# Kernel optimization log

Hardware: AMD Instinct MI355X
Metric: run time of the kernel (lower is better)

The kernel has to match this reference:

```python
import jax, jax.numpy as jnp
import numpy as np

T, B, IN, H, OUT, L = 2048, 16, 72, 256, 90, 2


def setup_inputs() -> dict:
    key = jax.random.key(0)
    ks = jax.random.split(key, 12)
    s = 0.05
    x = jax.random.normal(ks[0], (T, B, IN), jnp.float32)
    lengths = jnp.clip(jax.random.randint(ks[1], (B,), 1, T + 1), 1, T)
    W1 = jax.random.normal(ks[2], (H, IN), jnp.float32) * s
    b1 = jax.random.normal(ks[3], (H,), jnp.float32) * s
    Wih = jax.random.normal(ks[4], (L, 4 * H, H), jnp.float32) * s
    Whh = jax.random.normal(ks[5], (L, 4 * H, H), jnp.float32) * s
    bih = jax.random.normal(ks[6], (L, 4 * H), jnp.float32) * s
    bhh = jax.random.normal(ks[7], (L, 4 * H), jnp.float32) * s
    W2 = jax.random.normal(ks[8], (OUT, H), jnp.float32) * s
    b2 = jax.random.normal(ks[9], (OUT,), jnp.float32) * s
    return dict(x=x, lengths=lengths, W1=W1, b1=b1, Wih=Wih, Whh=Whh,
                bih=bih, bhh=bhh, W2=W2, b2=b2)


def _lstm_layer(x, mask, Wih, Whh, bih, bhh):
    # x: [T,B,H], mask: [T,B] bool (True = valid frame)
    Hh = Whh.shape[1]
    Bsz = x.shape[1]
    # input projection for all timesteps at once (the only big GEMM)
    gi = jnp.einsum('tbi,gi->tbg', x, Wih) + bih  # [T,B,4H]

    def step(carry, inp):
        h, c = carry
        g_in, m = inp
        g = g_in + h @ Whh.T + bhh
        i, f, gg, o = jnp.split(g, 4, axis=-1)  # PyTorch gate order i,f,g,o
        c_new = jax.nn.sigmoid(f) * c + jax.nn.sigmoid(i) * jnp.tanh(gg)
        h_new = jax.nn.sigmoid(o) * jnp.tanh(c_new)
        m2 = m[:, None]
        # pack semantics: state frozen past each sequence's length, output zero
        h = jnp.where(m2, h_new, h)
        c = jnp.where(m2, c_new, c)
        return (h, c), jnp.where(m2, h_new, jnp.zeros_like(h_new))

    init = (jnp.zeros((Bsz, Hh), x.dtype), jnp.zeros((Bsz, Hh), x.dtype))
    _, ys = jax.lax.scan(step, init, (gi, mask))
    return ys


def reference(x, lengths, W1, b1, Wih, Whh, bih, bhh, W2, b2):
    # linear1 + relu (dropout=0 -> identity)
    h = jax.nn.relu(jnp.einsum('tbi,hi->tbh', x, W1) + b1)
    mask = jnp.arange(T)[:, None] < lengths[None, :]  # [T,B]
    for l in range(L):
        h = _lstm_layer(h, mask, Wih[l], Whh[l], bih[l], bhh[l])
    y = jnp.einsum('tbh,oh->tbo', h, W2) + b2
    # zero out padded frames (they are discarded by the per-sequence slicing)
    return jnp.where(mask[:, :, None], y, jnp.zeros_like(y))
```

## Files before the change

### kernel.cpp

```cpp
#include <hip/hip_runtime.h>
#include <hip/hip_bf16.h>

#define T_STEPS 2048
#define HID 256
#define INF 72
#define OUTF 90
#define HSTR 528

typedef __attribute__((ext_vector_type(4))) float f32x4;
typedef __attribute__((ext_vector_type(8))) short s16x8;
typedef unsigned long long u64;

__device__ __forceinline__ unsigned short f2bf(float f) {
  union { float f; unsigned u; } v; v.f = f;
  unsigned r = (v.u + 0x7FFFu + ((v.u >> 16) & 1u)) >> 16;
  return (unsigned short)r;
}
__device__ __forceinline__ float bf2f(unsigned short s) {
  union { unsigned u; float f; } v; v.u = ((unsigned)s) << 16;
  return v.f;
}
__device__ __forceinline__ float sigm(float x) {
  return __builtin_amdgcn_rcpf(1.f + __builtin_amdgcn_exp2f(-1.44269504f * x));
}
__device__ __forceinline__ float tanh_f(float x) {
  return 1.f - 2.f * __builtin_amdgcn_rcpf(1.f + __builtin_amdgcn_exp2f(2.88539008f * x));
}

__device__ __forceinline__ u64 ld64(const u64* p) {
  return __hip_atomic_load(p, __ATOMIC_RELAXED, __HIP_MEMORY_SCOPE_AGENT);
}
__device__ __forceinline__ void st64(u64* p, u64 v) {
  __hip_atomic_store(p, v, __ATOMIC_RELAXED, __HIP_MEMORY_SCOPE_AGENT);
}
__device__ __forceinline__ void stflag(unsigned* p, unsigned v) {
  __hip_atomic_store(p, v, __ATOMIC_RELAXED, __HIP_MEMORY_SCOPE_AGENT);
}
__device__ __forceinline__ unsigned ldflag(const unsigned* p) {
  return __hip_atomic_load(p, __ATOMIC_RELAXED, __HIP_MEMORY_SCOPE_AGENT);
}
__device__ __forceinline__ void waitflag(const unsigned* p, unsigned target) {
  while (ldflag(p) < target) __builtin_amdgcn_s_sleep(1);
}
__device__ __forceinline__ unsigned wait2(const unsigned* creds, unsigned target, unsigned cred) {
  const u64* cp = (const u64*)creds;
  while (cred < target) {
    u64 v = ld64(cp);
    unsigned a = (unsigned)v, b = (unsigned)(v >> 32);
    cred = a < b ? a : b;
    if (cred < target) __builtin_amdgcn_s_sleep(2);
  }
  return cred;
}
__device__ __forceinline__ s16x8 ld16B_sc1(const unsigned short* p) {
  union { u64 u[2]; s16x8 v; } x;
  const u64* q = (const u64*)p;
  x.u[0] = ld64(q); x.u[1] = ld64(q + 1);
  return x.v;
}
template <int ROLE> __device__ __forceinline__ void ld_g(const unsigned short* p, s16x8& a, s16x8& b) {
  if constexpr (ROLE == 0) { a = *(const s16x8*)p; b = *(const s16x8*)(p + 8); }
  else {
    union { u64 u[2]; s16x8 v; } x, y;
    const u64* q = (const u64*)p;
    x.u[0] = ld64(q); x.u[1] = ld64(q + 1);
    y.u[0] = ld64(q + 2); y.u[1] = ld64(q + 3);
    a = x.v; b = y.v;
  }
}

__global__ __launch_bounds__(256) void inproj(const float* __restrict__ x,
                                              const float* __restrict__ W1,
                                              const float* __restrict__ b1,
                                              float* __restrict__ h0) {
  __shared__ float w1s[HID][INF + 1];
  __shared__ float xs[16][INF];
  const int tid = threadIdx.x;
  const int r0 = blockIdx.x * 16;
  for (int i = tid; i < HID * INF; i += 256) w1s[i / INF][i % INF] = W1[i];
  for (int i = tid; i < 16 * INF; i += 256)
    xs[i / INF][i % INF] = x[(size_t)(r0 + i / INF) * INF + (i % INF)];
  __syncthreads();
  const float bj = b1[tid];
  for (int r = 0; r < 16; ++r) {
    float acc = bj;
#pragma unroll 8
    for (int k = 0; k < INF; ++k) acc += xs[r][k] * w1s[tid][k];
    h0[(size_t)(r0 + r) * HID + tid] = fmaxf(acc, 0.f);
  }
}

__global__ __launch_bounds__(256) void wpack(const float* __restrict__ w,
                                             unsigned short* __restrict__ o) {
  const size_t i = ((size_t)blockIdx.x * 256 + threadIdx.x) * 8;
  f32x4 a = *(const f32x4*)(w + i);
  f32x4 b = *(const f32x4*)(w + i + 4);
  s16x8 v;
#pragma unroll
  for (int e = 0; e < 4; ++e) { v[e] = (short)f2bf(a[e]); v[4 + e] = (short)f2bf(b[e]); }
  *(s16x8*)(o + i) = v;
}

__global__ __launch_bounds__(256) void gi_mfma(const float* __restrict__ h,
                                               const unsigned short* __restrict__ wb,
                                               const float* __restrict__ bih,
                                               const float* __restrict__ bhh,
                                               unsigned short* __restrict__ gi) {
  __shared__ __align__(16) char hs[16 * HSTR];
  __shared__ float bs[1024];
  const int tid = threadIdx.x;
  const int t = blockIdx.x;
  const int lane = tid & 63;
  const int wg = tid >> 6;
  const int j = lane & 15;
  const int hi = lane >> 4;
  for (int i = tid; i < 1024; i += 256) bs[i] = bih[i] + bhh[i];
  {
    const int row = tid >> 4;
    const int c0 = (tid & 15) * 16;
    const float* src = h + ((size_t)t * 16 + row) * 256 + c0;
    f32x4 v0 = *(const f32x4*)(src);
    f32x4 v1 = *(const f32x4*)(src + 4);
    f32x4 v2 = *(const f32x4*)(src + 8);
    f32x4 v3 = *(const f32x4*)(src + 12);
    s16x8 p0, p1;
#pragma unroll
    for (int e = 0; e < 4; ++e) {
      p0[e] = (short)f2bf(v0[e]); p0[4 + e] = (short)f2bf(v1[e]);
      p1[e] = (short)f2bf(v2[e]); p1[4 + e] = (short)f2bf(v3[e]);
    }
    *(s16x8*)(hs + row * HSTR + c0 * 2) = p0;
    *(s16x8*)(hs + row * HSTR + c0 * 2 + 16) = p1;
  }
  __syncthreads();
  const int hread = j * HSTR + hi * 16;
  f32x4 acc[4][4] = {};
#pragma unroll
  for (int kt = 0; kt < 8; ++kt) {
    const int k = kt * 32 + hi * 8;
    const s16x8 a = *(const s16x8*)(hs + hread + kt * 64);
#pragma unroll
    for (int ug2 = 0; ug2 < 4; ++ug2)
#pragma unroll
      for (int q = 0; q < 4; ++q) {
        const s16x8 bw = *(const s16x8*)(wb + (((size_t)(q << 8) + wg * 64 + ug2 * 16 + j) << 8) + k);
        acc[ug2][q] = __builtin_amdgcn_mfma_f32_16x16x32_bf16(bw, a, acc[ug2][q], 0, 0, 0);
      }
  }
#pragma unroll
  for (int ug2 = 0; ug2 < 4; ++ug2) {
    const int sw = wg * 4 + ug2;
    const int uT = sw * 16 + hi * 4;
    s16x8 o0, o1;
#pragma unroll
    for (int r = 0; r < 4; ++r) {
      o0[r]     = (short)f2bf(acc[ug2][0][r] + bs[uT + r]);
      o0[4 + r] = (short)f2bf(acc[ug2][1][r] + bs[256 + uT + r]);
      o1[r]     = (short)f2bf(acc[ug2][2][r] + bs[512 + uT + r]);
      o1[4 + r] = (short)f2bf(acc[ug2][3][r] + bs[768 + uT + r]);
    }
    unsigned short* dst = gi + ((size_t)(t * 16 + sw) * 64 + lane) * 16;
    *(s16x8*)(dst) = o0;
    *(s16x8*)(dst + 8) = o1;
  }
}


template <int ROLE>
__device__ __forceinline__ void scan_tp(
    const unsigned short* __restrict__ gi,
    const unsigned short* __restrict__ whbL,
    const int* __restrict__ lengths,
    unsigned short* __restrict__ hb1,
    float* __restrict__ hout,
    unsigned short* hx,
    unsigned* myflag, unsigned* peerflag,
    unsigned* mycred,
    unsigned* creds,
    int half)
{
  __shared__ __align__(16) char hl[4 * 8192];
  const int tid  = threadIdx.x;
  const int lane = tid & 63;
  const int w    = tid >> 6;
  const int j    = lane & 15;
  const int hi   = lane >> 4;
  const int uB   = half * 128 + w * 16;
  const int myu  = uB + hi * 4;

  s16x8 wfr[32];
#pragma unroll
  for (int kt = 0; kt < 8; ++kt)
#pragma unroll
    for (int q = 0; q < 4; ++q)
      wfr[kt * 4 + q] =
          *(const s16x8*)(whbL + ((size_t)(q * 256 + uB + j) << 8) + kt * 32 + hi * 8);

  const int len = lengths[j];
  float c[4] = {};
  unsigned short hprev[4] = {};

  const int lws = ((j << 9) + (myu << 1)) ^ ((j & 7) << 4);
  *(u64*)(hl + lws) = 0;
  st64((u64*)hx + ((j * 256 + myu) >> 2), 0);
  asm volatile("s_waitcnt vmcnt(0) lgkmcnt(0)" ::: "memory");
  __builtin_amdgcn_s_barrier();
  if (tid == 0) stflag(myflag, 1u);

  const unsigned short* gp = gi + ((size_t)(half * 8 + w) * 64 + lane) * 16;
  unsigned cred = 0;
  if (ROLE == 1) cred = wait2(creds, 8u, cred);
  s16x8 gE0, gE1, gO0, gO1;
  ld_g<ROLE>(gp, gE0, gE1);
  ld_g<ROLE>(gp + 16384, gO0, gO1);

  const int pbase = (1 - half) * 128;

  for (int tg = 0; tg < T_STEPS; tg += 4) {
    if (ROLE == 1) {
      const unsigned target = (tg + 8 <= T_STEPS) ? (unsigned)(tg + 8) : (unsigned)T_STEPS;
      cred = wait2(creds, target, cred);
    }
#pragma unroll
    for (int ts = 0; ts < 4; ++ts) {
      const int t = tg + ts;
      s16x8& g0 = (ts & 1) ? gO0 : gE0;
      s16x8& g1 = (ts & 1) ? gO1 : gE1;
      const int cur = t & 3, nxt = (t + 1) & 3;

      waitflag(peerflag, (unsigned)(t + 1));

      s16x8 avp[4];
#pragma unroll
      for (int p = 0; p < 4; ++p) {
        const int k = pbase + p * 32 + hi * 8;
        avp[p] = ld16B_sc1(hx + cur * 4096 + j * 256 + k);
      }
      s16x8 avo[4];
#pragma unroll
      for (int p = 0; p < 4; ++p) {
        const int k = half * 128 + p * 32 + hi * 8;
        const int off = cur * 8192 + (((j << 9) + (k << 1)) ^ ((j & 7) << 4));
        avo[p] = *(const s16x8*)(hl + off);
      }

      f32x4 acc[4];
#pragma unroll
      for (int r = 0; r < 4; ++r) {
        acc[0][r] = bf2f((unsigned short)g0[r]);
        acc[1][r] = bf2f((unsigned short)g0[4 + r]);
        acc[2][r] = bf2f((unsigned short)g1[r]);
        acc[3][r] = bf2f((unsigned short)g1[4 + r]);
      }
#pragma unroll
      for (int kt = 0; kt < 8; ++kt) {
        const s16x8 a = ((kt >> 2) == half) ? avo[kt & 3] : avp[kt & 3];
#pragma unroll
        for (int q = 0; q < 4; ++q)
          acc[q] = __builtin_amdgcn_mfma_f32_16x16x32_bf16(wfr[kt * 4 + q], a, acc[q], 0, 0, 0);
      }

      u64 hpk = 0, ypk = 0;
      f32x4 yv;
      const bool m = t < len;
#pragma unroll
      for (int r = 0; r < 4; ++r) {
        const float i_  = sigm(acc[0][r]);
        const float f_  = sigm(acc[1][r]);
        const float tg_ = tanh_f(acc[2][r]);
        const float o_  = sigm(acc[3][r]);
        const float cn = f_ * c[r] + i_ * tg_;
        const float hv = o_ * tanh_f(cn);
        c[r] = m ? cn : c[r];
        const unsigned short hb = m ? f2bf(hv) : hprev[r];
        hprev[r] = hb;
        hpk |= (u64)hb << (16 * r);
        if (ROLE == 0) ypk |= (u64)(m ? hb : (unsigned short)0) << (16 * r);
        else           yv[r] = m ? hv : 0.f;
      }
      *(u64*)(hl + nxt * 8192 + lws) = hpk;
      st64((u64*)hx + ((nxt * 4096 + j * 256 + myu) >> 2), hpk);
      asm volatile("s_waitcnt vmcnt(0) lgkmcnt(0)" ::: "memory");
      __builtin_amdgcn_s_barrier();
      if (tid == 0) stflag(myflag, (unsigned)(t + 2));
      if (ROLE == 0) st64((u64*)hb1 + (((size_t)t * 4096 + j * 256 + myu) >> 2), ypk);
      else           *(f32x4*)(hout + ((size_t)t * 16 + j) * 256 + myu) = yv;
      {
        const int tn = (t + 2 < T_STEPS) ? t + 2 : T_STEPS - 1;
        ld_g<ROLE>(gp + (size_t)tn * 16384, g0, g1);
      }
    }
    if (ROLE == 0) {
      asm volatile("s_waitcnt vmcnt(0)" ::: "memory");
      __builtin_amdgcn_s_barrier();
      if (tid == 0) stflag(mycred, (unsigned)(tg + 4));
    }
  }
}

__device__ __forceinline__ void gi2b(int cu,
    const unsigned short* __restrict__ hb1,
    const unsigned short* __restrict__ wb2,
    const float* __restrict__ bih2, const float* __restrict__ bhh2,
    unsigned short* __restrict__ gf2,
    unsigned* creds_in, unsigned* mycred)
{
  const int tid = threadIdx.x;
  const int lane = tid & 63;
  const int w = tid >> 6;
  const int j = lane & 15;
  const int hi = lane >> 4;
  const int sw = cu * 8 + w;

  s16x8 wfr[32];
  float bsum[4][4];
#pragma unroll
  for (int kt = 0; kt < 8; ++kt)
#pragma unroll
    for (int q = 0; q < 4; ++q)
      wfr[kt * 4 + q] =
          *(const s16x8*)(wb2 + ((size_t)(q * 256 + sw * 16 + j) << 8) + kt * 32 + hi * 8);
#pragma unroll
  for (int q = 0; q < 4; ++q)
#pragma unroll
    for (int r = 0; r < 4; ++r) {
      const int col = q * 256 + sw * 16 + hi * 4 + r;
      bsum[q][r] = bih2[col] + bhh2[col];
    }

  unsigned cred = 0;
  for (int tg = 0; tg < T_STEPS; tg += 4) {
    cred = wait2(creds_in, (unsigned)(tg + 4), cred);
#pragma unroll
    for (int ts = 0; ts < 4; ++ts) {
      const int t = tg + ts;
      const unsigned short* ab = hb1 + (size_t)t * 4096 + j * 256 + hi * 8;
      s16x8 av[8];
#pragma unroll
      for (int kt = 0; kt < 8; ++kt) av[kt] = ld16B_sc1(ab + kt * 32);
      f32x4 acc[4];
#pragma unroll
      for (int q = 0; q < 4; ++q)
#pragma unroll
        for (int r = 0; r < 4; ++r) acc[q][r] = bsum[q][r];
#pragma unroll
      for (int kt = 0; kt < 8; ++kt)
#pragma unroll
        for (int q = 0; q < 4; ++q)
          acc[q] = __builtin_amdgcn_mfma_f32_16x16x32_bf16(wfr[kt * 4 + q], av[kt], acc[q], 0, 0, 0);
      u64 p0 = 0, q0 = 0, p1 = 0, q1 = 0;
#pragma unroll
      for (int r = 0; r < 4; ++r) {
        p0 |= (u64)f2bf(acc[0][r]) << (16 * r);
        q0 |= (u64)f2bf(acc[1][r]) << (16 * r);
        p1 |= (u64)f2bf(acc[2][r]) << (16 * r);
        q1 |= (u64)f2bf(acc[3][r]) << (16 * r);
      }
      u64* dst = (u64*)gf2 + ((size_t)(t * 16 + sw) * 64 + lane) * 4;
      st64(dst, p0); st64(dst + 1, q0); st64(dst + 2, p1); st64(dst + 3, q1);
    }
    asm volatile("s_waitcnt vmcnt(0)" ::: "memory");
    __builtin_amdgcn_s_barrier();
    if (tid == 0) stflag(mycred, (unsigned)(tg + 4));
  }
}

__global__ __launch_bounds__(512, 2) void fused_pipe(
    const unsigned short* __restrict__ gf1,
    const unsigned short* __restrict__ whb,
    const unsigned short* __restrict__ wb,
    const float* __restrict__ bih, const float* __restrict__ bhh,
    const int* __restrict__ lengths,
    unsigned short* hb1, unsigned short* gf2, float* hout2,
    unsigned short* hx1, unsigned short* hx2, unsigned* sync)
{
  const int bid = blockIdx.x;
  if (bid == 0)
    scan_tp<0>(gf1, whb, lengths, hb1, nullptr, hx1, sync + 0, sync + 1, sync + 8, nullptr, 0);
  else if (bid == 1)
    scan_tp<0>(gf1, whb, lengths, hb1, nullptr, hx1, sync + 1, sync + 0, sync + 9, nullptr, 1);
  else if (bid == 2)
    gi2b(0, hb1, wb + 262144, bih + 1024, bhh + 1024, gf2, sync + 8, sync + 12);
  else if (bid == 3)
    gi2b(1, hb1, wb + 262144, bih + 1024, bhh + 1024, gf2, sync + 8, sync + 13);
  else if (bid == 4)
    scan_tp<1>(gf2, whb + 262144, lengths, nullptr, hout2, hx2, sync + 2, sync + 3, nullptr, sync + 12, 0);
  else
    scan_tp<1>(gf2, whb + 262144, lengths, nullptr, hout2, hx2, sync + 3, sync + 2, nullptr, sync + 12, 1);
}

__global__ __launch_bounds__(256) void outproj(const float* __restrict__ h2,
                                               const float* __restrict__ W2,
                                               const float* __restrict__ b2,
                                               const int* __restrict__ lengths,
                                               float* __restrict__ y) {
  __shared__ float w2s[OUTF][HID + 1];
  __shared__ float hs[8][HID + 1];
  const int tid = threadIdx.x;
  const int r0 = blockIdx.x * 8;
  for (int i = tid; i < OUTF * HID; i += 256) w2s[i / HID][i % HID] = W2[i];
  for (int i = tid; i < 8 * HID; i += 256)
    hs[i / HID][i % HID] = h2[(size_t)(r0 + i / HID) * HID + (i % HID)];
  __syncthreads();
  for (int oi = tid; oi < 8 * OUTF; oi += 256) {
    const int r = oi / OUTF, o = oi % OUTF;
    const int row = r0 + r, t = row >> 4, b = row & 15;
    float acc = b2[o];
#pragma unroll 8
    for (int k = 0; k < HID; ++k) acc += hs[r][k] * w2s[o][k];
    y[(size_t)row * OUTF + o] = (t < lengths[b]) ? acc : 0.f;
  }
}

extern "C" void kernel_launch(void* const* d_in, const int* in_sizes, int n_in,
                              void* d_out, int out_size, void* d_ws, size_t ws_size,
                              hipStream_t stream) {
  const float* x      = (const float*)d_in[0];
  const int*   lengths= (const int*)d_in[1];
  const float* W1     = (const float*)d_in[2];
  const float* b1     = (const float*)d_in[3];
  const float* Wih    = (const float*)d_in[4];
  const float* Whh    = (const float*)d_in[5];
  const float* bih    = (const float*)d_in[6];
  const float* bhh    = (const float*)d_in[7];
  const float* W2     = (const float*)d_in[8];
  const float* b2     = (const float*)d_in[9];
  float* out = (float*)d_out;

  char* ws = (char*)d_ws;
  float*          h0   = (float*)(ws);
  unsigned short* gf1  = (unsigned short*)(ws + 33554432);
  unsigned short* hb1  = (unsigned short*)(ws + 100663296);
  unsigned short* gf2  = (unsigned short*)(ws + 117440512);
  float*          h2o  = (float*)(ws + 184549376);
  unsigned short* wb   = (unsigned short*)(ws + 218103808);
  unsigned short* whb  = (unsigned short*)(ws + 219152384);
  unsigned short* hx1  = (unsigned short*)(ws + 220200960);
  unsigned short* hx2  = (unsigned short*)(ws + 220233728);
  unsigned*       sync = (unsigned*)(ws + 220266496);

  wpack<<<256, 256, 0, stream>>>(Wih, wb);
  wpack<<<256, 256, 0, stream>>>(Whh, whb);
  inproj<<<2048, 256, 0, stream>>>(x, W1, b1, h0);
  gi_mfma<<<2048, 256, 0, stream>>>(h0, wb, bih, bhh, gf1);

  hipMemsetAsync((void*)hx1, 0, 2 * 32768 + 1024, stream);
  fused_pipe<<<6, 512, 0, stream>>>(gf1, whb, wb, bih, bhh, lengths,
                                    hb1, gf2, h2o, hx1, hx2, sync);

  outproj<<<4096, 256, 0, stream>>>(h2o, W2, b2, lengths, out);
}
```

Measured before the change: 9.317 ms.

## Replace per-step flag handshake with tagged hidden-state exchange between scan blocks

The two blocks that split each LSTM layer's hidden units no longer signal each step with a flag store and poll. Each 32-bit pair of bf16 h values is now stored alongside a 32-bit timestep tag in one 64-bit atomic word, and the consumer polls the data itself until all tags match. It computes the local half of the recurrent matmul from LDS before spinning on the peer half, and issues the next gate-input prefetch earlier. This removes the per-step global store drain and flag round trip, at the cost of doubling exchange buffer size and traffic and relying on 64-bit store atomicity.

```diff
diff --git a/kernel.cpp b/kernel.cpp
--- a/kernel.cpp
+++ b/kernel.cpp
@@ -35,12 +35,6 @@
 }
 __device__ __forceinline__ void stflag(unsigned* p, unsigned v) {
   __hip_atomic_store(p, v, __ATOMIC_RELAXED, __HIP_MEMORY_SCOPE_AGENT);
-}
-__device__ __forceinline__ unsigned ldflag(const unsigned* p) {
-  return __hip_atomic_load(p, __ATOMIC_RELAXED, __HIP_MEMORY_SCOPE_AGENT);
-}
-__device__ __forceinline__ void waitflag(const unsigned* p, unsigned target) {
-  while (ldflag(p) < target) __builtin_amdgcn_s_sleep(1);
 }
 __device__ __forceinline__ unsigned wait2(const unsigned* creds, unsigned target, unsigned cred) {
   const u64* cp = (const u64*)creds;
@@ -52,21 +46,8 @@
   }
   return cred;
 }
-__device__ __forceinline__ s16x8 ld16B_sc1(const unsigned short* p) {
-  union { u64 u[2]; s16x8 v; } x;
-  const u64* q = (const u64*)p;
-  x.u[0] = ld64(q); x.u[1] = ld64(q + 1);
-  return x.v;
-}
-template <int ROLE> __device__ __forceinline__ void ld_g(const unsigned short* p, s16x8& a, s16x8& b) {
-  if constexpr (ROLE == 0) { a = *(const s16x8*)p; b = *(const s16x8*)(p + 8); }
-  else {
-    union { u64 u[2]; s16x8 v; } x, y;
-    const u64* q = (const u64*)p;
-    x.u[0] = ld64(q); x.u[1] = ld64(q + 1);
-    y.u[0] = ld64(q + 2); y.u[1] = ld64(q + 3);
-    a = x.v; b = y.v;
-  }
+__device__ __forceinline__ void ld_g(const unsigned short* p, s16x8& a, s16x8& b) {
+  a = *(const s16x8*)p; b = *(const s16x8*)(p + 8);
 }
 
 __global__ __launch_bounds__(256) void inproj(const float* __restrict__ x,
@@ -173,8 +154,7 @@
     const int* __restrict__ lengths,
     unsigned short* __restrict__ hb1,
     float* __restrict__ hout,
-    unsigned short* hx,
-    unsigned* myflag, unsigned* peerflag,
+    u64* hx,
     unsigned* mycred,
     unsigned* creds,
     int half)
@@ -202,17 +182,15 @@
 
   const int lws = ((j << 9) + (myu << 1)) ^ ((j & 7) << 4);
   *(u64*)(hl + lws) = 0;
-  st64((u64*)hx + ((j * 256 + myu) >> 2), 0);
-  asm volatile("s_waitcnt vmcnt(0) lgkmcnt(0)" ::: "memory");
+  asm volatile("s_waitcnt lgkmcnt(0)" ::: "memory");
   __builtin_amdgcn_s_barrier();
-  if (tid == 0) stflag(myflag, 1u);
 
   const unsigned short* gp = gi + ((size_t)(half * 8 + w) * 64 + lane) * 16;
   unsigned cred = 0;
   if (ROLE == 1) cred = wait2(creds, 8u, cred);
   s16x8 gE0, gE1, gO0, gO1;
-  ld_g<ROLE>(gp, gE0, gE1);
-  ld_g<ROLE>(gp + 16384, gO0, gO1);
+  ld_g(gp, gE0, gE1);
+  ld_g(gp + 16384, gO0, gO1);
 
   const int pbase = (1 - half) * 128;
 
@@ -228,22 +206,6 @@
       s16x8& g1 = (ts & 1) ? gO1 : gE1;
       const int cur = t & 3, nxt = (t + 1) & 3;
 
-      waitflag(peerflag, (unsigned)(t + 1));
-
-      s16x8 avp[4];
-#pragma unroll
-      for (int p = 0; p < 4; ++p) {
-        const int k = pbase + p * 32 + hi * 8;
-        avp[p] = ld16B_sc1(hx + cur * 4096 + j * 256 + k);
-      }
-      s16x8 avo[4];
-#pragma unroll
-      for (int p = 0; p < 4; ++p) {
-        const int k = half * 128 + p * 32 + hi * 8;
-        const int off = cur * 8192 + (((j << 9) + (k << 1)) ^ ((j & 7) << 4));
-        avo[p] = *(const s16x8*)(hl + off);
-      }
-
       f32x4 acc[4];
 #pragma unroll
       for (int r = 0; r < 4; ++r) {
@@ -252,12 +214,52 @@
         acc[2][r] = bf2f((unsigned short)g1[r]);
         acc[3][r] = bf2f((unsigned short)g1[4 + r]);
       }
-#pragma unroll
-      for (int kt = 0; kt < 8; ++kt) {
-        const s16x8 a = ((kt >> 2) == half) ? avo[kt & 3] : avp[kt & 3];
+      {
+        const int tn = (t + 2 < T_STEPS) ? t + 2 : T_STEPS - 1;
+        ld_g(gp + (size_t)tn * 16384, g0, g1);
+      }
+
+#pragma unroll
+      for (int p = 0; p < 4; ++p) {
+        const int kt = half * 4 + p;
+        const int k = half * 128 + p * 32 + hi * 8;
+        const int off = cur * 8192 + (((j << 9) + (k << 1)) ^ ((j & 7) << 4));
+        const s16x8 a = *(const s16x8*)(hl + off);
 #pragma unroll
         for (int q = 0; q < 4; ++q)
           acc[q] = __builtin_amdgcn_mfma_f32_16x16x32_bf16(wfr[kt * 4 + q], a, acc[q], 0, 0, 0);
+      }
+
+      s16x8 avp[4];
+      {
+        const unsigned tagexp = (unsigned)t;
+        for (;;) {
+          bool ok = true;
+#pragma unroll
+          for (int p = 0; p < 4; ++p) {
+            const int k = pbase + p * 32 + hi * 8;
+            const u64* src = hx + (size_t)cur * 2048 + j * 128 + (k >> 1);
+            const u64 a0 = ld64(src), a1 = ld64(src + 1);
+            const u64 a2 = ld64(src + 2), a3 = ld64(src + 3);
+            ok &= ((unsigned)(a0 >> 32) == tagexp) & ((unsigned)(a1 >> 32) == tagexp) &
+                  ((unsigned)(a2 >> 32) == tagexp) & ((unsigned)(a3 >> 32) == tagexp);
+            s16x8 v;
+            v[0] = (short)a0; v[1] = (short)(a0 >> 16);
+            v[2] = (short)a1; v[3] = (short)(a1 >> 16);
+            v[4] = (short)a2; v[5] = (short)(a2 >> 16);
+            v[6] = (short)a3; v[7] = (short)(a3 >> 16);
+            avp[p] = v;
+          }
+          if (__ballot((int)ok) == ~0ull) break;
+          __builtin_amdgcn_s_sleep(1);
+        }
+      }
+#pragma unroll
+      for (int p = 0; p < 4; ++p) {
+        const int kt = (1 - half) * 4 + p;
+#pragma unroll
+        for (int q = 0; q < 4; ++q)
+          acc[q] = __builtin_amdgcn_mfma_f32_16x16x32_bf16(wfr[kt * 4 + q], avp[p], acc[q], 0, 0, 0);
       }
 
       u64 hpk = 0, ypk = 0;
@@ -279,21 +281,24 @@
         else           yv[r] = m ? hv : 0.f;
       }
       *(u64*)(hl + nxt * 8192 + lws) = hpk;
-      st64((u64*)hx + ((nxt * 4096 + j * 256 + myu) >> 2), hpk);
-      asm volatile("s_waitcnt vmcnt(0) lgkmcnt(0)" ::: "memory");
-      __builtin_amdgcn_s_barrier();
-      if (tid == 0) stflag(myflag, (unsigned)(t + 2));
+      {
+        const u64 tag = (u64)(unsigned)(t + 1) << 32;
+        u64* dst = hx + (size_t)nxt * 2048 + j * 128 + (myu >> 1);
+        st64(dst,     (hpk & 0xFFFFFFFFull) | tag);
+        st64(dst + 1, (hpk >> 32)           | tag);
+      }
       if (ROLE == 0) st64((u64*)hb1 + (((size_t)t * 4096 + j * 256 + myu) >> 2), ypk);
       else           *(f32x4*)(hout + ((size_t)t * 16 + j) * 256 + myu) = yv;
-      {
-        const int tn = (t + 2 < T_STEPS) ? t + 2 : T_STEPS - 1;
-        ld_g<ROLE>(gp + (size_t)tn * 16384, g0, g1);
-      }
-    }
-    if (ROLE == 0) {
-      asm volatile("s_waitcnt vmcnt(0)" ::: "memory");
-      __builtin_amdgcn_s_barrier();
-      if (tid == 0) stflag(mycred, (unsigned)(tg + 4));
+
+      if (ROLE == 0 && ts == 3) {
+        asm volatile("s_waitcnt vmcnt(0) lgkmcnt(0)" ::: "memory");
+        __builtin_amdgcn_s_barrier();
+        if (tid == 0) stflag(mycred, (unsigned)(tg + 4));
+      } else {
+        asm volatile("s_waitcnt lgkmcnt(0)" ::: "memory");
+        __builtin_amdgcn_s_barrier();
+      }
+      asm volatile("" ::: "memory");
     }
   }
 }
@@ -337,7 +342,7 @@
       const unsigned short* ab = hb1 + (size_t)t * 4096 + j * 256 + hi * 8;
       s16x8 av[8];
 #pragma unroll
-      for (int kt = 0; kt < 8; ++kt) av[kt] = ld16B_sc1(ab + kt * 32);
+      for (int kt = 0; kt < 8; ++kt) av[kt] = *(const s16x8*)(ab + kt * 32);
       f32x4 acc[4];
 #pragma unroll
       for (int q = 0; q < 4; ++q)
@@ -372,21 +377,21 @@
     const float* __restrict__ bih, const float* __restrict__ bhh,
     const int* __restrict__ lengths,
     unsigned short* hb1, unsigned short* gf2, float* hout2,
-    unsigned short* hx1, unsigned short* hx2, unsigned* sync)
+    u64* hx1, u64* hx2, unsigned* sync)
 {
   const int bid = blockIdx.x;
   if (bid == 0)
-    scan_tp<0>(gf1, whb, lengths, hb1, nullptr, hx1, sync + 0, sync + 1, sync + 8, nullptr, 0);
+    scan_tp<0>(gf1, whb, lengths, hb1, nullptr, hx1, sync + 8, nullptr, 0);
   else if (bid == 1)
-    scan_tp<0>(gf1, whb, lengths, hb1, nullptr, hx1, sync + 1, sync + 0, sync + 9, nullptr, 1);
+    scan_tp<0>(gf1, whb, lengths, hb1, nullptr, hx1, sync + 9, nullptr, 1);
   else if (bid == 2)
     gi2b(0, hb1, wb + 262144, bih + 1024, bhh + 1024, gf2, sync + 8, sync + 12);
   else if (bid == 3)
     gi2b(1, hb1, wb + 262144, bih + 1024, bhh + 1024, gf2, sync + 8, sync + 13);
   else if (bid == 4)
-    scan_tp<1>(gf2, whb + 262144, lengths, nullptr, hout2, hx2, sync + 2, sync + 3, nullptr, sync + 12, 0);
+    scan_tp<1>(gf2, whb + 262144, lengths, nullptr, hout2, hx2, nullptr, sync + 12, 0);
   else
-    scan_tp<1>(gf2, whb + 262144, lengths, nullptr, hout2, hx2, sync + 3, sync + 2, nullptr, sync + 12, 1);
+    scan_tp<1>(gf2, whb + 262144, lengths, nullptr, hout2, hx2, nullptr, sync + 12, 1);
 }
 
 __global__ __launch_bounds__(256) void outproj(const float* __restrict__ h2,
@@ -435,16 +440,16 @@
   float*          h2o  = (float*)(ws + 184549376);
   unsigned short* wb   = (unsigned short*)(ws + 218103808);
   unsigned short* whb  = (unsigned short*)(ws + 219152384);
-  unsigned short* hx1  = (unsigned short*)(ws + 220200960);
-  unsigned short* hx2  = (unsigned short*)(ws + 220233728);
-  unsigned*       sync = (unsigned*)(ws + 220266496);
+  u64*            hx1  = (u64*)(ws + 220200960);
+  u64*            hx2  = (u64*)(ws + 220266496);
+  unsigned*       sync = (unsigned*)(ws + 220332032);
 
   wpack<<<256, 256, 0, stream>>>(Wih, wb);
   wpack<<<256, 256, 0, stream>>>(Whh, whb);
   inproj<<<2048, 256, 0, stream>>>(x, W1, b1, h0);
   gi_mfma<<<2048, 256, 0, stream>>>(h0, wb, bih, bhh, gf1);
 
-  hipMemsetAsync((void*)hx1, 0, 2 * 32768 + 1024, stream);
+  hipMemsetAsync((void*)hx1, 0, 2 * 65536 + 1024, stream);
   fused_pipe<<<6, 512, 0, stream>>>(gf1, whb, wb, bih, bhh, lengths,
                                     hb1, gf2, h2o, hx1, hx2, sync);
 
```

New measurement: 15.82 ms. 69.8% more time.

## Run each LSTM layer scan on one CU and add clock-keeper blocks

Applied to the files above, without the earlier changes.

Each layer's recurrent scan moves from two cooperating workgroups, which traded hidden state through global memory with per-step flags, to a single 512-thread workgroup. That workgroup keeps most of Whh in registers and 144KB of dynamic LDS and streams the remaining weight tiles from global memory every step. The goal is to remove the per-timestep cross-CU flag handshake and global round trip from the critical path. In exchange, each CU does twice the MFMA work per step and carries heavier register and LDS pressure. The grid also grows to 200 blocks; the extra blocks run a 'keeper' loop of dummy FMAs until the layer-2 scan signals completion, apparently to hold the GPU busy and clocked up.

```diff
diff --git a/kernel.cpp b/kernel.cpp
--- a/kernel.cpp
+++ b/kernel.cpp
@@ -6,6 +6,8 @@
 #define INF 72
 #define OUTF 90
 #define HSTR 528
+#define VT 32
+#define LT 18
 
 typedef __attribute__((ext_vector_type(4))) float f32x4;
 typedef __attribute__((ext_vector_type(8))) short s16x8;
@@ -40,7 +42,7 @@
   return __hip_atomic_load(p, __ATOMIC_RELAXED, __HIP_MEMORY_SCOPE_AGENT);
 }
 __device__ __forceinline__ void waitflag(const unsigned* p, unsigned target) {
-  while (ldflag(p) < target) __builtin_amdgcn_s_sleep(1);
+  while (ldflag(p) < target) __builtin_amdgcn_s_sleep(2);
 }
 __device__ __forceinline__ unsigned wait2(const unsigned* creds, unsigned target, unsigned cred) {
   const u64* cp = (const u64*)creds;
@@ -166,136 +168,158 @@
 }
 
 
+#define SKT(i) (((50 + (i)) >> 2) - 8)
+#define SQ(i)  ((50 + (i)) & 3)
+
 template <int ROLE>
-__device__ __forceinline__ void scan_tp(
+__device__ __forceinline__ void scan_1cu(
     const unsigned short* __restrict__ gi,
     const unsigned short* __restrict__ whbL,
     const int* __restrict__ lengths,
     unsigned short* __restrict__ hb1,
     float* __restrict__ hout,
-    unsigned short* hx,
-    unsigned* myflag, unsigned* peerflag,
     unsigned* mycred,
     unsigned* creds,
-    int half)
+    char* smem)
 {
-  __shared__ __align__(16) char hl[4 * 8192];
-  const int tid  = threadIdx.x;
+  char* wl = smem;
+  char* hl = smem + 147456;
+  const int tid = threadIdx.x;
   const int lane = tid & 63;
-  const int w    = tid >> 6;
-  const int j    = lane & 15;
-  const int hi   = lane >> 4;
-  const int uB   = half * 128 + w * 16;
-  const int myu  = uB + hi * 4;
-
-  s16x8 wfr[32];
-#pragma unroll
-  for (int kt = 0; kt < 8; ++kt)
-#pragma unroll
-    for (int q = 0; q < 4; ++q)
-      wfr[kt * 4 + q] =
-          *(const s16x8*)(whbL + ((size_t)(q * 256 + uB + j) << 8) + kt * 32 + hi * 8);
+  const int w = tid >> 6;
+  const int j = lane & 15;
+  const int hi = lane >> 4;
+
+  s16x8 wfr[VT];
+#pragma unroll
+  for (int ug = 0; ug < 2; ++ug)
+#pragma unroll
+    for (int kt = 0; kt < 8; ++kt)
+#pragma unroll
+      for (int q = 0; q < 4; ++q) {
+        const int tau = (ug * 8 + kt) * 4 + q;
+        if (tau >= VT + LT) continue;
+        const int row = q * 256 + w * 32 + ug * 16 + j;
+        const s16x8 v = *(const s16x8*)(whbL + ((size_t)row << 8) + kt * 32 + hi * 8);
+        if (tau < VT) wfr[tau] = v;
+        else *(s16x8*)(wl + (w * LT + (tau - VT)) * 1024 + lane * 16) = v;
+      }
+  for (int i = tid; i < 2048; i += 512) ((float*)hl)[i] = 0.f;
 
   const int len = lengths[j];
-  float c[4] = {};
-  unsigned short hprev[4] = {};
-
-  const int lws = ((j << 9) + (myu << 1)) ^ ((j & 7) << 4);
-  *(u64*)(hl + lws) = 0;
-  st64((u64*)hx + ((j * 256 + myu) >> 2), 0);
-  asm volatile("s_waitcnt vmcnt(0) lgkmcnt(0)" ::: "memory");
-  __builtin_amdgcn_s_barrier();
-  if (tid == 0) stflag(myflag, 1u);
-
-  const unsigned short* gp = gi + ((size_t)(half * 8 + w) * 64 + lane) * 16;
+  float c[8] = {};
+  unsigned short hprev[8] = {};
+  __syncthreads();
+
+  const unsigned short* gp = gi + ((size_t)(w * 2) * 64 + lane) * 16;
+  const unsigned short* swp = whbL + (size_t)(w * 32 + 16 + j) * 256 + hi * 8;
+
   unsigned cred = 0;
   if (ROLE == 1) cred = wait2(creds, 8u, cred);
-  s16x8 gE0, gE1, gO0, gO1;
-  ld_g<ROLE>(gp, gE0, gE1);
-  ld_g<ROLE>(gp + 16384, gO0, gO1);
-
-  const int pbase = (1 - half) * 128;
+  s16x8 gE[4], gO[4];
+  ld_g<ROLE>(gp, gE[0], gE[1]);
+  ld_g<ROLE>(gp + 1024, gE[2], gE[3]);
+
+  auto STEP = [&](int t, s16x8 (&gc)[4], s16x8 (&gn)[4]) {
+    const int cur = t & 1, nxt = cur ^ 1;
+    {
+      const int tn = (t + 1 < T_STEPS) ? t + 1 : t;
+      const unsigned short* np = gp + (size_t)tn * 16384;
+      ld_g<ROLE>(np, gn[0], gn[1]);
+      ld_g<ROLE>(np + 1024, gn[2], gn[3]);
+    }
+    s16x8 gw[14];
+#pragma unroll
+    for (int i = 0; i < 5; ++i) gw[i] = *(const s16x8*)(swp + SQ(i) * 65536 + SKT(i) * 32);
+
+    f32x4 acc0[4], acc1[4];
+#pragma unroll
+    for (int r = 0; r < 4; ++r) {
+      acc0[0][r] = bf2f((unsigned short)gc[0][r]);
+      acc0[1][r] = bf2f((unsigned short)gc[0][4 + r]);
+      acc0[2][r] = bf2f((unsigned short)gc[1][r]);
+      acc0[3][r] = bf2f((unsigned short)gc[1][4 + r]);
+      acc1[0][r] = bf2f((unsigned short)gc[2][r]);
+      acc1[1][r] = bf2f((unsigned short)gc[2][4 + r]);
+      acc1[2][r] = bf2f((unsigned short)gc[3][r]);
+      acc1[3][r] = bf2f((unsigned short)gc[3][4 + r]);
+    }
+#pragma unroll
+    for (int kt = 0; kt < 8; ++kt) {
+      const int hoff = cur * 8192 + (((j << 9) + ((kt * 32 + hi * 8) << 1)) ^ ((j & 7) << 4));
+      const s16x8 a = *(const s16x8*)(hl + hoff);
+#pragma unroll
+      for (int q = 0; q < 4; ++q)
+        acc0[q] = __builtin_amdgcn_mfma_f32_16x16x32_bf16(wfr[kt * 4 + q], a, acc0[q], 0, 0, 0);
+#pragma unroll
+      for (int q = 0; q < 4; ++q) {
+        const int tau = 32 + kt * 4 + q;
+        s16x8 bw;
+        if (tau < VT + LT) bw = *(const s16x8*)(wl + (w * LT + (tau - VT)) * 1024 + lane * 16);
+        else bw = gw[tau - 50];
+        acc1[q] = __builtin_amdgcn_mfma_f32_16x16x32_bf16(bw, a, acc1[q], 0, 0, 0);
+      }
+      if (kt == 1) {
+#pragma unroll
+        for (int i = 5; i < 10; ++i) gw[i] = *(const s16x8*)(swp + SQ(i) * 65536 + SKT(i) * 32);
+      }
+      if (kt == 3) {
+#pragma unroll
+        for (int i = 10; i < 14; ++i) gw[i] = *(const s16x8*)(swp + SQ(i) * 65536 + SKT(i) * 32);
+      }
+    }
+    const bool m = t < len;
+#pragma unroll
+    for (int ug = 0; ug < 2; ++ug) {
+      const int u = w * 32 + ug * 16 + hi * 4;
+      u64 hpk = 0, ypk = 0;
+      f32x4 yv;
+#pragma unroll
+      for (int r = 0; r < 4; ++r) {
+        const int ci = ug * 4 + r;
+        const float a0 = ug ? acc1[0][r] : acc0[0][r];
+        const float a1 = ug ? acc1[1][r] : acc0[1][r];
+        const float a2 = ug ? acc1[2][r] : acc0[2][r];
+        const float a3 = ug ? acc1[3][r] : acc0[3][r];
+        const float i_  = sigm(a0);
+        const float f_  = sigm(a1);
+        const float tg_ = tanh_f(a2);
+        const float o_  = sigm(a3);
+        const float cn = f_ * c[ci] + i_ * tg_;
+        const float hv = o_ * tanh_f(cn);
+        c[ci] = m ? cn : c[ci];
+        const unsigned short hb = m ? f2bf(hv) : hprev[ci];
+        hprev[ci] = hb;
+        hpk |= (u64)hb << (16 * r);
+        if (ROLE == 0) ypk |= (u64)(m ? hb : (unsigned short)0) << (16 * r);
+        else           yv[r] = m ? hv : 0.f;
+      }
+      *(u64*)(hl + nxt * 8192 + (((j << 9) + (u << 1)) ^ ((j & 7) << 4))) = hpk;
+      if (ROLE == 0) st64((u64*)hb1 + (((size_t)t * 4096 + j * 256 + u) >> 2), ypk);
+      else           *(f32x4*)(hout + ((size_t)t * 16 + j) * 256 + u) = yv;
+    }
+    if (ROLE == 0 && (t & 3) == 3) {
+      asm volatile("s_waitcnt vmcnt(0) lgkmcnt(0)" ::: "memory");
+      __builtin_amdgcn_s_barrier();
+      if (tid == 0) stflag(mycred, (unsigned)(t + 1));
+    } else {
+      asm volatile("s_waitcnt lgkmcnt(0)" ::: "memory");
+      __builtin_amdgcn_s_barrier();
+    }
+    asm volatile("" ::: "memory");
+  };
 
   for (int tg = 0; tg < T_STEPS; tg += 4) {
     if (ROLE == 1) {
       const unsigned target = (tg + 8 <= T_STEPS) ? (unsigned)(tg + 8) : (unsigned)T_STEPS;
       cred = wait2(creds, target, cred);
     }
-#pragma unroll
-    for (int ts = 0; ts < 4; ++ts) {
-      const int t = tg + ts;
-      s16x8& g0 = (ts & 1) ? gO0 : gE0;
-      s16x8& g1 = (ts & 1) ? gO1 : gE1;
-      const int cur = t & 3, nxt = (t + 1) & 3;
-
-      waitflag(peerflag, (unsigned)(t + 1));
-
-      s16x8 avp[4];
-#pragma unroll
-      for (int p = 0; p < 4; ++p) {
-        const int k = pbase + p * 32 + hi * 8;
-        avp[p] = ld16B_sc1(hx + cur * 4096 + j * 256 + k);
-      }
-      s16x8 avo[4];
-#pragma unroll
-      for (int p = 0; p < 4; ++p) {
-        const int k = half * 128 + p * 32 + hi * 8;
-        const int off = cur * 8192 + (((j << 9) + (k << 1)) ^ ((j & 7) << 4));
-        avo[p] = *(const s16x8*)(hl + off);
-      }
-
-      f32x4 acc[4];
-#pragma unroll
-      for (int r = 0; r < 4; ++r) {
-        acc[0][r] = bf2f((unsigned short)g0[r]);
-        acc[1][r] = bf2f((unsigned short)g0[4 + r]);
-        acc[2][r] = bf2f((unsigned short)g1[r]);
-        acc[3][r] = bf2f((unsigned short)g1[4 + r]);
-      }
-#pragma unroll
-      for (int kt = 0; kt < 8; ++kt) {
-        const s16x8 a = ((kt >> 2) == half) ? avo[kt & 3] : avp[kt & 3];
-#pragma unroll
-        for (int q = 0; q < 4; ++q)
-          acc[q] = __builtin_amdgcn_mfma_f32_16x16x32_bf16(wfr[kt * 4 + q], a, acc[q], 0, 0, 0);
-      }
-
-      u64 hpk = 0, ypk = 0;
-      f32x4 yv;
-      const bool m = t < len;
-#pragma unroll
-      for (int r = 0; r < 4; ++r) {
-        const float i_  = sigm(acc[0][r]);
-        const float f_  = sigm(acc[1][r]);
-        const float tg_ = tanh_f(acc[2][r]);
-        const float o_  = sigm(acc[3][r]);
-        const float cn = f_ * c[r] + i_ * tg_;
-        const float hv = o_ * tanh_f(cn);
-        c[r] = m ? cn : c[r];
-        const unsigned short hb = m ? f2bf(hv) : hprev[r];
-        hprev[r] = hb;
-        hpk |= (u64)hb << (16 * r);
-        if (ROLE == 0) ypk |= (u64)(m ? hb : (unsigned short)0) << (16 * r);
-        else           yv[r] = m ? hv : 0.f;
-      }
-      *(u64*)(hl + nxt * 8192 + lws) = hpk;
-      st64((u64*)hx + ((nxt * 4096 + j * 256 + myu) >> 2), hpk);
-      asm volatile("s_waitcnt vmcnt(0) lgkmcnt(0)" ::: "memory");
-      __builtin_amdgcn_s_barrier();
-      if (tid == 0) stflag(myflag, (unsigned)(t + 2));
-      if (ROLE == 0) st64((u64*)hb1 + (((size_t)t * 4096 + j * 256 + myu) >> 2), ypk);
-      else           *(f32x4*)(hout + ((size_t)t * 16 + j) * 256 + myu) = yv;
-      {
-        const int tn = (t + 2 < T_STEPS) ? t + 2 : T_STEPS - 1;
-        ld_g<ROLE>(gp + (size_t)tn * 16384, g0, g1);
-      }
-    }
-    if (ROLE == 0) {
-      asm volatile("s_waitcnt vmcnt(0)" ::: "memory");
-      __builtin_amdgcn_s_barrier();
-      if (tid == 0) stflag(mycred, (unsigned)(tg + 4));
-    }
-  }
+    STEP(tg,     gE, gO);
+    STEP(tg + 1, gO, gE);
+    STEP(tg + 2, gE, gO);
+    STEP(tg + 3, gO, gE);
+  }
+  if (ROLE == 1 && tid == 0) stflag(mycred, 1u);
 }
 
 __device__ __forceinline__ void gi2b(int cu,
@@ -303,7 +327,7 @@
     const unsigned short* __restrict__ wb2,
     const float* __restrict__ bih2, const float* __restrict__ bhh2,
     unsigned short* __restrict__ gf2,
-    unsigned* creds_in, unsigned* mycred)
+    unsigned* cred_in, unsigned* mycred)
 {
   const int tid = threadIdx.x;
   const int lane = tid & 63;
@@ -328,9 +352,8 @@
       bsum[q][r] = bih2[col] + bhh2[col];
     }
 
-  unsigned cred = 0;
   for (int tg = 0; tg < T_STEPS; tg += 4) {
-    cred = wait2(creds_in, (unsigned)(tg + 4), cred);
+    waitflag(cred_in, (unsigned)(tg + 4));
 #pragma unroll
     for (int ts = 0; ts < 4; ++ts) {
       const int t = tg + ts;
@@ -363,6 +386,22 @@
     __builtin_amdgcn_s_barrier();
     if (tid == 0) stflag(mycred, (unsigned)(tg + 4));
   }
+}
+
+__device__ __forceinline__ void keeper(const unsigned* donef, const float* junk) {
+  float a = (float)(threadIdx.x + 1) * 1e-12f;
+  const float b = 1.0000001f;
+  for (int it = 0; it < 40000; ++it) {
+    unsigned d = 0;
+    if ((threadIdx.x & 63) == 0) d = ldflag(donef);
+    d = (unsigned)__shfl((int)d, 0, 64);
+    if (d) break;
+    const int idx = (it * 12289 + (int)(blockIdx.x * 512u + threadIdx.x)) & 8388607;
+    a += junk[idx] * 1e-30f;
+#pragma unroll 32
+    for (int i = 0; i < 2048; ++i) a = __builtin_fmaf(a, b, 1e-20f);
+  }
+  asm volatile("" :: "v"(a));
 }
 
 __global__ __launch_bounds__(512, 2) void fused_pipe(
@@ -372,21 +411,20 @@
     const float* __restrict__ bih, const float* __restrict__ bhh,
     const int* __restrict__ lengths,
     unsigned short* hb1, unsigned short* gf2, float* hout2,
-    unsigned short* hx1, unsigned short* hx2, unsigned* sync)
+    const float* __restrict__ junk, unsigned* sync)
 {
+  extern __shared__ char smem[];
   const int bid = blockIdx.x;
   if (bid == 0)
-    scan_tp<0>(gf1, whb, lengths, hb1, nullptr, hx1, sync + 0, sync + 1, sync + 8, nullptr, 0);
+    scan_1cu<0>(gf1, whb, lengths, hb1, nullptr, sync + 8, nullptr, smem);
   else if (bid == 1)
-    scan_tp<0>(gf1, whb, lengths, hb1, nullptr, hx1, sync + 1, sync + 0, sync + 9, nullptr, 1);
+    gi2b(0, hb1, wb + 262144, bih + 1024, bhh + 1024, gf2, sync + 8, sync + 12);
   else if (bid == 2)
-    gi2b(0, hb1, wb + 262144, bih + 1024, bhh + 1024, gf2, sync + 8, sync + 12);
+    gi2b(1, hb1, wb + 262144, bih + 1024, bhh + 1024, gf2, sync + 8, sync + 13);
   else if (bid == 3)
-    gi2b(1, hb1, wb + 262144, bih + 1024, bhh + 1024, gf2, sync + 8, sync + 13);
-  else if (bid == 4)
-    scan_tp<1>(gf2, whb + 262144, lengths, nullptr, hout2, hx2, sync + 2, sync + 3, nullptr, sync + 12, 0);
+    scan_1cu<1>(gf2, whb + 262144, lengths, nullptr, hout2, sync + 20, sync + 12, smem);
   else
-    scan_tp<1>(gf2, whb + 262144, lengths, nullptr, hout2, hx2, sync + 3, sync + 2, nullptr, sync + 12, 1);
+    keeper(sync + 20, junk);
 }
 
 __global__ __launch_bounds__(256) void outproj(const float* __restrict__ h2,
@@ -435,18 +473,19 @@
   float*          h2o  = (float*)(ws + 184549376);
   unsigned short* wb   = (unsigned short*)(ws + 218103808);
   unsigned short* whb  = (unsigned short*)(ws + 219152384);
-  unsigned short* hx1  = (unsigned short*)(ws + 220200960);
-  unsigned short* hx2  = (unsigned short*)(ws + 220233728);
   unsigned*       sync = (unsigned*)(ws + 220266496);
+
+  hipFuncSetAttribute((const void*)fused_pipe,
+                      hipFuncAttributeMaxDynamicSharedMemorySize, 163840);
 
   wpack<<<256, 256, 0, stream>>>(Wih, wb);
   wpack<<<256, 256, 0, stream>>>(Whh, whb);
   inproj<<<2048, 256, 0, stream>>>(x, W1, b1, h0);
   gi_mfma<<<2048, 256, 0, stream>>>(h0, wb, bih, bhh, gf1);
 
-  hipMemsetAsync((void*)hx1, 0, 2 * 32768 + 1024, stream);
-  fused_pipe<<<6, 512, 0, stream>>>(gf1, whb, wb, bih, bhh, lengths,
-                                    hb1, gf2, h2o, hx1, hx2, sync);
+  hipMemsetAsync((void*)sync, 0, 1024, stream);
+  fused_pipe<<<200, 512, 163840, stream>>>(gf1, whb, wb, bih, bhh, lengths,
+                                           hb1, gf2, h2o, h0, sync);
 
   outproj<<<4096, 256, 0, stream>>>(h2o, W2, b2, lengths, out);
 }
```

Result: slower. 15.59 ms (+67.3%).
